# Performance work log

Measured on AMD Instinct MI355X. Metric: run time of the kernel, lower is better.

The kernel has to match this reference:

```python
import jax, jax.numpy as jnp
import numpy as np

N_NODES = 100000
E2 = 1600000
E3 = 1600000
ES = 100000
HID = 64


def _mlp_3x3(x_in, W1, b1, W2, b2):
    # x_in: [E, d_in] -> mobility [E, 3, 3]
    h = jax.nn.relu(x_in @ W1 + b1)
    out = h @ W2 + b2  # [E, 9]
    return out.reshape(-1, 3, 3)


def setup_inputs() -> dict:
    key = jax.random.key(0)
    ks = jax.random.split(key, 20)
    inp = {}
    inp["x"] = jax.random.normal(ks[0], (N_NODES, 3), dtype=jnp.float32)
    inp["edge_2body"] = jax.random.randint(ks[1], (2, E2), 0, N_NODES)
    inp["edge_3body"] = jax.random.randint(ks[2], (3, E3), 0, N_NODES)
    inp["edge_2bodySelf"] = jax.random.randint(ks[3], (2, ES), 0, N_NODES)
    inp["edge_1body"] = jax.random.randint(ks[4], (2, ES), 0, N_NODES)
    inp["edge_attr_2body"] = jax.random.normal(ks[5], (E2, 3), dtype=jnp.float32)
    inp["edge_attr_3body"] = jax.random.normal(ks[6], (E3, 3), dtype=jnp.float32)
    inp["edge_attr_2bodySelf"] = jax.random.normal(ks[7], (ES, 3), dtype=jnp.float32)
    inp["edge_attr_1body"] = jax.random.normal(ks[8], (ES, 3), dtype=jnp.float32)
    s = 0.1
    # nn_2body: 3 -> HID -> 9
    inp["W1_2b"] = jax.random.normal(ks[9], (3, HID), dtype=jnp.float32) * s
    inp["b1_2b"] = jnp.zeros((HID,), jnp.float32)
    inp["W2_2b"] = jax.random.normal(ks[10], (HID, 9), dtype=jnp.float32) * s
    inp["b2_2b"] = jnp.zeros((9,), jnp.float32)
    # nn_3body: 6 -> HID -> 9
    inp["W1_3b"] = jax.random.normal(ks[11], (6, HID), dtype=jnp.float32) * s
    inp["b1_3b"] = jnp.zeros((HID,), jnp.float32)
    inp["W2_3b"] = jax.random.normal(ks[12], (HID, 9), dtype=jnp.float32) * s
    inp["b2_3b"] = jnp.zeros((9,), jnp.float32)
    # nn_self: 3 -> HID -> 9
    inp["W1_s"] = jax.random.normal(ks[13], (3, HID), dtype=jnp.float32) * s
    inp["b1_s"] = jnp.zeros((HID,), jnp.float32)
    inp["W2_s"] = jax.random.normal(ks[14], (HID, 9), dtype=jnp.float32) * s
    inp["b2_s"] = jnp.zeros((9,), jnp.float32)
    return inp


def reference(x, edge_2body, edge_3body, edge_2bodySelf, edge_1body,
              edge_attr_2body, edge_attr_3body, edge_attr_2bodySelf, edge_attr_1body,
              W1_2b, b1_2b, W2_2b, b2_2b,
              W1_3b, b1_3b, W2_3b, b2_3b,
              W1_s, b1_s, W2_s, b2_s):
    n = x.shape[0]
    # ---- 2-body: gather -> MLP -> per-edge 3x3 matvec -> scatter-add ----
    d2 = x[edge_2body[0]] - x[edge_2body[1]]  # xj - xi, [E2,3]
    mob2 = _mlp_3x3(d2, W1_2b, b1_2b, W2_2b, b2_2b)
    y2 = jnp.einsum('eij,ej->ei', mob2, edge_attr_2body)
    v2 = jax.ops.segment_sum(y2, edge_2body[1], num_segments=n)
    # ---- 3-body ----
    xj = x[edge_3body[0]]
    xk = x[edge_3body[1]]
    xi = x[edge_3body[2]]
    d3 = jnp.concatenate((xk - xj, xi - xk), axis=1)  # [E3,6]
    mob3 = _mlp_3x3(d3, W1_3b, b1_3b, W2_3b, b2_3b)
    y3 = jnp.einsum('eij,ej->ei', mob3, edge_attr_3body)
    v3 = jax.ops.segment_sum(y3, edge_3body[2], num_segments=n)
    # ---- 2-body self ----
    ds = x[edge_2bodySelf[0]] - x[edge_2bodySelf[1]]
    mobs = _mlp_3x3(ds, W1_s, b1_s, W2_s, b2_s)
    ys = jnp.einsum('eij,ej->ei', mobs, edge_attr_2bodySelf)
    vs = jax.ops.segment_sum(ys, edge_2bodySelf[1], num_segments=n)
    # edge_1body / edge_attr_1body unused in original forward
    return v2 + v3 + vs
```

## Files before the change

kernel.cpp:

```cpp
#include <hip/hip_runtime.h>


constexpr int HIDDEN = 64;
constexpr int NB_MAX = 256;
constexpr int NPB_SHIFT = 9;
constexpr int NPB = 1 << NPB_SHIFT;
constexpr int TILE_F = NPB * 3;
constexpr int NET_SLOT = 1040;
constexpr int BLK = 256;
constexpr int KPT = 4;

typedef _Float16 h2_t __attribute__((ext_vector_type(2)));

__device__ __forceinline__ unsigned packh2(float a, float b) {
    auto h = __builtin_amdgcn_cvt_pkrtz(a, b);
    return __builtin_bit_cast(unsigned, h);
}
__device__ __forceinline__ float fdot2u(unsigned a, unsigned b, float c) {
    h2_t ha = __builtin_bit_cast(h2_t, a);
    h2_t hb = __builtin_bit_cast(h2_t, b);
#if __has_builtin(__builtin_amdgcn_fdot2)
    return __builtin_amdgcn_fdot2(ha, hb, c, false);
#else
    return fmaf((float)ha.x, (float)hb.x, fmaf((float)ha.y, (float)hb.y, c));
#endif
}


__global__ __launch_bounds__(256) void setup_kernel(
    const float* __restrict__ x, int n_nodes, float4* __restrict__ x4,
    int* __restrict__ gcount,
    const float* __restrict__ W1_2b, const float* __restrict__ b1_2b,
    const float* __restrict__ W2_2b, const float* __restrict__ b2_2b,
    const float* __restrict__ W1_s,  const float* __restrict__ b1_s,
    const float* __restrict__ W2_s,  const float* __restrict__ b2_s,
    const float* __restrict__ W1_3b, const float* __restrict__ b1_3b,
    const float* __restrict__ W2_3b, const float* __restrict__ b2_3b,
    unsigned* __restrict__ nets)
{
    const int blk = blockIdx.x;
    const int tid = threadIdx.x;
    if (blk < 3) {
        const float *W1, *b1, *W2, *b2; int din;
        if (blk == 0) { W1 = W1_2b; b1 = b1_2b; W2 = W2_2b; b2 = b2_2b; din = 3; }
        else if (blk == 1) { W1 = W1_s; b1 = b1_s; W2 = W2_s; b2 = b2_s; din = 3; }
        else { W1 = W1_3b; b1 = b1_3b; W2 = W2_3b; b2 = b2_3b; din = 6; }
        unsigned* slot = nets + blk * NET_SLOT;
        float* slotf = (float*)slot;
        if (tid < 32) {
            const int h2 = tid, hA = 2 * h2, hB = 2 * h2 + 1;
            if (din == 3) {
                unsigned* row = slot + h2 * 16;
                float* rowf = (float*)row;
                row[0] = packh2(W1[0 * HIDDEN + hA], W1[1 * HIDDEN + hA]);
                row[1] = packh2(W1[0 * HIDDEN + hB], W1[1 * HIDDEN + hB]);
                rowf[2] = b1[hA]; rowf[3] = b1[hB];
                rowf[4] = W1[2 * HIDDEN + hA]; rowf[5] = W1[2 * HIDDEN + hB];
                #pragma unroll
                for (int i = 0; i < 9; ++i)
                    row[6 + i] = packh2(W2[hA * 9 + i], W2[hB * 9 + i]);
                row[15] = 0;
            } else {
                unsigned* row = slot + h2 * 32;
                float* rowf = (float*)row;
                #pragma unroll
                for (int r = 0; r < 3; ++r) {
                    row[r]     = packh2(W1[(2 * r) * HIDDEN + hA], W1[(2 * r + 1) * HIDDEN + hA]);
                    row[3 + r] = packh2(W1[(2 * r) * HIDDEN + hB], W1[(2 * r + 1) * HIDDEN + hB]);
                }
                rowf[6] = b1[hA]; rowf[7] = b1[hB];
                #pragma unroll
                for (int i = 0; i < 9; ++i)
                    row[8 + i] = packh2(W2[hA * 9 + i], W2[hB * 9 + i]);
                #pragma unroll
                for (int i = 17; i < 20; ++i) row[i] = 0;
            }
        }
        if (tid >= 32 && tid < 41) slotf[1024 + (tid - 32)] = b2[tid - 32];
        if (blk == 0) gcount[tid] = 0;
    } else {
        int i = (blk - 3) * 256 + tid;
        if (i < n_nodes)
            x4[i] = make_float4(x[3 * i], x[3 * i + 1], x[3 * i + 2], 0.0f);
    }
}

__global__ __launch_bounds__(256) void p1_edge_kernel(
    const float4* __restrict__ x4,
    const int* __restrict__ e0, long long E0, const float* __restrict__ at0,
    const int* __restrict__ e1, long long E1, const float* __restrict__ at1,
    const int* __restrict__ e2, long long E2, const float* __restrict__ at2,
    int g0, int g1,
    const unsigned* __restrict__ nets,
    float4* __restrict__ records, int* __restrict__ gcount, int cap)
{
    static_assert(NB_MAX == BLK, "one reserve bin per thread");
    __shared__ __align__(16) unsigned s_net[1033];
    __shared__ int s_rank[NB_MAX];
    __shared__ int s_base[NB_MAX];

    const int gA = g0 + g1;
    const int gB = (int)gridDim.x - gA;
    const int mn = (gA < gB) ? gA : gB;
    int aidx = -1, b6 = -1;
    {
        const int idx = blockIdx.x;
        if (idx < 2 * mn) { if (idx & 1) b6 = idx >> 1; else aidx = idx >> 1; }
        else {
            const int r = idx - 2 * mn;
            if (gA > gB) aidx = mn + r; else b6 = mn + r;
        }
    }

    const int* edges; long long E; const float* attr;
    int bidx, nblk, din3;
    const unsigned* wp;
    if (aidx >= 0) {
        if (aidx < g0) { edges = e0; E = E0; attr = at0; bidx = aidx;      nblk = g0; din3 = 1; wp = nets; }
        else           { edges = e1; E = E1; attr = at1; bidx = aidx - g0; nblk = g1; din3 = 1; wp = nets + NET_SLOT; }
    } else             { edges = e2; E = E2; attr = at2; bidx = b6;        nblk = gB; din3 = 0; wp = nets + 2 * NET_SLOT; }

    const int tid = threadIdx.x;
    long long span = (E + nblk - 1) / nblk;
    span = (span + 1023) & ~1023LL;
    const long long lo = (long long)bidx * span;
    const long long hi = (lo + span < E) ? (lo + span) : E;
    if (lo >= E) return;

    const bool e_aligned = ((E & 3) == 0);

    s_rank[tid] = 0;
    const int nstage = din3 ? 512 : 1024;
    for (int i = tid; i < nstage; i += BLK) s_net[i] = wp[i];
    if (tid < 9) s_net[1024 + tid] = wp[1024 + tid];
    __syncthreads();

    const unsigned* w = s_net;
    const float* wf = (const float*)s_net;
    float b2r[9];
    #pragma unroll
    for (int i = 0; i < 9; ++i) b2r[i] = wf[1024 + i];

    const long long be = lo + (long long)tid * KPT;

    unsigned dp[KPT][3];
    float    d2s[KPT];
    float    a[KPT][3];
    int      dst[KPT];
    bool     valid[KPT];
    int      i0[KPT], i1[KPT], i2[KPT];

    const bool lane_live = (be < hi);
    const bool full = lane_live && e_aligned && (be + KPT <= hi);
    if (full) {
        int4 r0 = *(const int4*)(edges + be);
        int4 r1 = *(const int4*)(edges + E + be);
        i0[0] = r0.x; i0[1] = r0.y; i0[2] = r0.z; i0[3] = r0.w;
        i1[0] = r1.x; i1[1] = r1.y; i1[2] = r1.z; i1[3] = r1.w;
        if (!din3) {
            int4 r2 = *(const int4*)(edges + 2 * E + be);
            i2[0] = r2.x; i2[1] = r2.y; i2[2] = r2.z; i2[3] = r2.w;
        }
        float4 a0 = *(const float4*)(attr + 3 * be);
        float4 a1 = *(const float4*)(attr + 3 * be + 4);
        float4 a2 = *(const float4*)(attr + 3 * be + 8);
        a[0][0] = a0.x; a[0][1] = a0.y; a[0][2] = a0.z;
        a[1][0] = a0.w; a[1][1] = a1.x; a[1][2] = a1.y;
        a[2][0] = a1.z; a[2][1] = a1.w; a[2][2] = a2.x;
        a[3][0] = a2.y; a[3][1] = a2.z; a[3][2] = a2.w;
        #pragma unroll
        for (int u = 0; u < KPT; ++u) valid[u] = true;
    } else {
        #pragma unroll
        for (int u = 0; u < KPT; ++u) {
            long long e = be + u;
            valid[u] = lane_live && (e < hi);
            long long ee = valid[u] ? e : lo;
            i0[u] = edges[ee];
            i1[u] = edges[E + ee];
            if (!din3) i2[u] = edges[2 * E + ee];
            #pragma unroll
            for (int c = 0; c < 3; ++c) a[u][c] = attr[3 * ee + c];
        }
    }

    #pragma unroll
    for (int u = 0; u < KPT; ++u) {
        if (din3) {
            dst[u] = i1[u];
            float4 xs = x4[i0[u]];
            float4 xt = x4[i1[u]];
            dp[u][0] = packh2(xs.x - xt.x, xs.y - xt.y);
            d2s[u]   = xs.z - xt.z;
            dp[u][1] = 0; dp[u][2] = 0;
        } else {
            dst[u] = i2[u];
            float4 xj = x4[i0[u]];
            float4 xk = x4[i1[u]];
            float4 xi = x4[i2[u]];
            dp[u][0] = packh2(xk.x - xj.x, xk.y - xj.y);
            dp[u][1] = packh2(xk.z - xj.z, xi.x - xk.x);
            dp[u][2] = packh2(xi.y - xk.y, xi.z - xk.z);
            d2s[u] = 0.f;
        }
    }

    float acc[KPT][9];
    #pragma unroll
    for (int u = 0; u < KPT; ++u)
        #pragma unroll
        for (int i = 0; i < 9; ++i) acc[u][i] = b2r[i];

    if (din3) {
        #pragma unroll 2
        for (int hh2 = 0; hh2 < HIDDEN / 2; ++hh2) {
            const uint4* rq = (const uint4*)(w + (hh2 << 4));
            const uint4 q0 = rq[0], q1 = rq[1], q2 = rq[2], q3 = rq[3];
            const unsigned wA = q0.x;
            const unsigned wB = q0.y;
            const float bbA = __uint_as_float(q0.z);
            const float bbB = __uint_as_float(q0.w);
            const float wcA = __uint_as_float(q1.x);
            const float wcB = __uint_as_float(q1.y);
            const unsigned w2p[9] = {q1.z, q1.w, q2.x, q2.y, q2.z,
                                     q2.w, q3.x, q3.y, q3.z};
            #pragma unroll
            for (int u = 0; u < KPT; ++u) {
                float preA = fmaf(d2s[u], wcA, fdot2u(dp[u][0], wA, bbA));
                float preB = fmaf(d2s[u], wcB, fdot2u(dp[u][0], wB, bbB));
                unsigned h2 = packh2(fmaxf(preA, 0.f), fmaxf(preB, 0.f));
                #pragma unroll
                for (int i = 0; i < 9; ++i)
                    acc[u][i] = fdot2u(h2, w2p[i], acc[u][i]);
            }
        }
    } else {
        #pragma unroll 2
        for (int hh2 = 0; hh2 < HIDDEN / 2; ++hh2) {
            const uint4* rq = (const uint4*)(w + (hh2 << 5));
            const uint4 q0 = rq[0], q1 = rq[1], q2 = rq[2], q3 = rq[3];
            const unsigned q4x = w[(hh2 << 5) + 16];
            const unsigned wA0 = q0.x, wA1 = q0.y, wA2 = q0.z;
            const unsigned wB0 = q0.w, wB1 = q1.x, wB2 = q1.y;
            const float bbA = __uint_as_float(q1.z);
            const float bbB = __uint_as_float(q1.w);
            const unsigned w2p[9] = {q2.x, q2.y, q2.z, q2.w, q3.x,
                                     q3.y, q3.z, q3.w, q4x};
            #pragma unroll
            for (int u = 0; u < KPT; ++u) {
                float preA = fdot2u(dp[u][2], wA2,
                             fdot2u(dp[u][1], wA1,
                             fdot2u(dp[u][0], wA0, bbA)));
                float preB = fdot2u(dp[u][2], wB2,
                             fdot2u(dp[u][1], wB1,
                             fdot2u(dp[u][0], wB0, bbB)));
                unsigned h2 = packh2(fmaxf(preA, 0.f), fmaxf(preB, 0.f));
                #pragma unroll
                for (int i = 0; i < 9; ++i)
                    acc[u][i] = fdot2u(h2, w2p[i], acc[u][i]);
            }
        }
    }

    int rk[KPT]; int bb[KPT];
    #pragma unroll
    for (int u = 0; u < KPT; ++u) {
        if (valid[u]) {
            bb[u] = dst[u] >> NPB_SHIFT;
            rk[u] = atomicAdd(&s_rank[bb[u]], 1);
        }
    }
    __syncthreads();

    {
        int c = s_rank[tid];
        s_base[tid] = (c > 0) ? atomicAdd(&gcount[tid], c) : 0;
    }
    __syncthreads();

    #pragma unroll
    for (int u = 0; u < KPT; ++u) {
        if (!valid[u]) continue;
        float y0 = fmaf(acc[u][0], a[u][0], fmaf(acc[u][1], a[u][1], acc[u][2] * a[u][2]));
        float y1 = fmaf(acc[u][3], a[u][0], fmaf(acc[u][4], a[u][1], acc[u][5] * a[u][2]));
        float y2 = fmaf(acc[u][6], a[u][0], fmaf(acc[u][7], a[u][1], acc[u][8] * a[u][2]));
        int slot = s_base[bb[u]] + rk[u];
        if (slot < cap)
            records[(size_t)bb[u] * cap + slot] =
                make_float4(y0, y1, y2, __int_as_float(dst[u]));
    }
}

__global__ __launch_bounds__(1024) void p2_bucket(
    const float4* __restrict__ records, const int* __restrict__ gcount,
    int cap, int n_nodes, float* __restrict__ out)
{
    __shared__ float s_acc[TILE_F];
    const int b = blockIdx.x;
    const int tid = threadIdx.x;

    for (int i = tid; i < TILE_F; i += 1024) s_acc[i] = 0.0f;
    __syncthreads();

    int cnt = gcount[b];
    if (cnt > cap) cnt = cap;
    const float4* rb = records + (size_t)b * cap;
    for (int i = tid; i < cnt; i += 1024) {
        float4 r = rb[i];
        int loc = __float_as_int(r.w) - (b << NPB_SHIFT);
        atomicAdd(&s_acc[loc * 3 + 0], r.x);
        atomicAdd(&s_acc[loc * 3 + 1], r.y);
        atomicAdd(&s_acc[loc * 3 + 2], r.z);
    }
    __syncthreads();

    const int start = (b << NPB_SHIFT) * 3;
    const int end = min(n_nodes * 3, ((b + 1) << NPB_SHIFT) * 3);
    for (int i = start + tid; i < end; i += 1024)
        out[i] = s_acc[i - start];
}

template <int DIN, int KPTF>
__global__ __launch_bounds__(256) void edge_mlp_atomic(
    const float* __restrict__ x,
    const int* __restrict__ edges, long long E,
    const float* __restrict__ attr,
    const float* __restrict__ W1, const float* __restrict__ b1,
    const float* __restrict__ W2, const float* __restrict__ b2,
    float* __restrict__ out)
{
    const int tid = threadIdx.x;
    const long long base = (long long)blockIdx.x * (blockDim.x * KPTF) + tid;
    float d[KPTF][DIN]; float a[KPTF][3]; int dst[KPTF]; bool valid[KPTF];
    #pragma unroll
    for (int u = 0; u < KPTF; ++u) {
        long long e = base + (long long)u * blockDim.x;
        valid[u] = (e < E);
        long long ee = valid[u] ? e : 0;
        if constexpr (DIN == 3) {
            int s = edges[ee]; int t = edges[E + ee]; dst[u] = t;
            #pragma unroll
            for (int c = 0; c < 3; ++c)
                d[u][c] = x[3 * (long long)s + c] - x[3 * (long long)t + c];
        } else {
            int j = edges[ee]; int k = edges[E + ee]; int i = edges[2 * E + ee];
            dst[u] = i;
            #pragma unroll
            for (int c = 0; c < 3; ++c) {
                float xj = x[3 * (long long)j + c];
                float xk = x[3 * (long long)k + c];
                float xi = x[3 * (long long)i + c];
                d[u][c] = xk - xj; d[u][3 + c] = xi - xk;
            }
        }
        #pragma unroll
        for (int c = 0; c < 3; ++c) a[u][c] = attr[3 * ee + c];
    }
    float acc[KPTF][9];
    #pragma unroll
    for (int u = 0; u < KPTF; ++u)
        #pragma unroll
        for (int i = 0; i < 9; ++i) acc[u][i] = b2[i];
    #pragma unroll 4
    for (int hh = 0; hh < HIDDEN; ++hh) {
        const float bb = b1[hh];
        float w1r[DIN];
        #pragma unroll
        for (int r = 0; r < DIN; ++r) w1r[r] = W1[r * HIDDEN + hh];
        float w2r[9];
        #pragma unroll
        for (int i = 0; i < 9; ++i) w2r[i] = W2[hh * 9 + i];
        #pragma unroll
        for (int u = 0; u < KPTF; ++u) {
            float pre = bb;
            #pragma unroll
            for (int r = 0; r < DIN; ++r) pre = fmaf(d[u][r], w1r[r], pre);
            const float h = fmaxf(pre, 0.0f);
            #pragma unroll
            for (int i = 0; i < 9; ++i) acc[u][i] = fmaf(h, w2r[i], acc[u][i]);
        }
    }
    #pragma unroll
    for (int u = 0; u < KPTF; ++u) {
        if (!valid[u]) continue;
        float* o = out + 3 * (long long)dst[u];
        #pragma unroll
        for (int i = 0; i < 3; ++i) {
            float y = fmaf(acc[u][3 * i + 0], a[u][0],
                      fmaf(acc[u][3 * i + 1], a[u][1],
                           acc[u][3 * i + 2] * a[u][2]));
            atomicAdd(&o[i], y);
        }
    }
}

extern "C" void kernel_launch(void* const* d_in, const int* in_sizes, int n_in,
                              void* d_out, int out_size, void* d_ws, size_t ws_size,
                              hipStream_t stream)
{
    const float* x  = (const float*)d_in[0];
    const int*   e2 = (const int*)d_in[1];
    const int*   e3 = (const int*)d_in[2];
    const int*   es = (const int*)d_in[3];
    const float* a2 = (const float*)d_in[5];
    const float* a3 = (const float*)d_in[6];
    const float* as = (const float*)d_in[7];
    const float* W1_2b = (const float*)d_in[9];
    const float* b1_2b = (const float*)d_in[10];
    const float* W2_2b = (const float*)d_in[11];
    const float* b2_2b = (const float*)d_in[12];
    const float* W1_3b = (const float*)d_in[13];
    const float* b1_3b = (const float*)d_in[14];
    const float* W2_3b = (const float*)d_in[15];
    const float* b2_3b = (const float*)d_in[16];
    const float* W1_s  = (const float*)d_in[17];
    const float* b1_s  = (const float*)d_in[18];
    const float* W2_s  = (const float*)d_in[19];
    const float* b2_s  = (const float*)d_in[20];

    const long long E2 = in_sizes[1] / 2;
    const long long E3 = in_sizes[2] / 3;
    const long long ES = in_sizes[3] / 2;
    const long long Etot = E2 + E3 + ES;
    const int n_nodes = out_size / 3;
    const int nbuckets = (n_nodes + NPB - 1) >> NPB_SHIFT;

    float* out = (float*)d_out;

    const size_t off_nets = 1024;
    const size_t off_x4 = (off_nets + 3 * NET_SLOT * 4 + 255) & ~(size_t)255;
    const size_t x4_bytes = (size_t)n_nodes * sizeof(float4);
    const size_t off_rec = (off_x4 + x4_bytes + 255) & ~(size_t)255;

    long long mean_per_bucket = (Etot + nbuckets - 1) / nbuckets;
    long long min_cap = mean_per_bucket + 1600;
    long long cap_avail =
        ((long long)ws_size - (long long)off_rec) / ((long long)nbuckets * 16);

    constexpr int SPAN = 1024;
    int g0 = (int)((E2 + SPAN - 1) / SPAN);
    int g1 = (int)((ES + SPAN - 1) / SPAN);
    int g2g = (int)((E3 + SPAN - 1) / SPAN);

    if (nbuckets <= NB_MAX && cap_avail >= min_cap) {
        long long capL = min_cap + 4096;
        if (capL > cap_avail) capL = cap_avail;
        int cap = (int)capL;
        int* gcount = (int*)d_ws;
        unsigned* nets = (unsigned*)((char*)d_ws + off_nets);
        float4* x4 = (float4*)((char*)d_ws + off_x4);
        float4* records = (float4*)((char*)d_ws + off_rec);

        int nb_pad = (n_nodes + 255) / 256;
        setup_kernel<<<3 + nb_pad, 256, 0, stream>>>(
            x, n_nodes, x4, gcount,
            W1_2b, b1_2b, W2_2b, b2_2b,
            W1_s,  b1_s,  W2_s,  b2_s,
            W1_3b, b1_3b, W2_3b, b2_3b,
            nets);

        p1_edge_kernel<<<g0 + g1 + g2g, 256, 0, stream>>>(
            x4,
            e2, E2, a2,
            es, ES, as,
            e3, E3, a3,
            g0, g1,
            nets, records, gcount, cap);

        p2_bucket<<<nbuckets, 1024, 0, stream>>>(records, gcount, cap, n_nodes, out);
    } else {
        hipMemsetAsync(out, 0, (size_t)out_size * sizeof(float), stream);
        constexpr int FB_BLK = 256, FB_KPT = 4;
        const long long per_blk = (long long)FB_BLK * FB_KPT;
        int a2g = (int)((E2 + per_blk - 1) / per_blk);
        int a3g = (int)((E3 + per_blk - 1) / per_blk);
        int asg = (int)((ES + per_blk - 1) / per_blk);
        if (a2g > 0)
            edge_mlp_atomic<3, FB_KPT><<<a2g, FB_BLK, 0, stream>>>(
                x, e2, E2, a2, W1_2b, b1_2b, W2_2b, b2_2b, out);
        if (a3g > 0)
            edge_mlp_atomic<6, FB_KPT><<<a3g, FB_BLK, 0, stream>>>(
                x, e3, E3, a3, W1_3b, b1_3b, W2_3b, b2_3b, out);
        if (asg > 0)
            edge_mlp_atomic<3, FB_KPT><<<asg, FB_BLK, 0, stream>>>(
                x, es, ES, as, W1_s, b1_s, W2_s, b2_s, out);
    }
}
```

Measured before the change: 285.4 us.

## Double edges per thread and privatize bucket accumulators per wavefront

Raises the number of edges each thread handles in the bucketing kernel from 4 to 8, widening the vector loads and halving the grid, so each shared-memory weight load is reused across more edges. The hidden-layer loops lose their unroll-by-2 pragma to limit register growth. The bucket reduce kernel now gives each of the 16 wavefronts its own shared accumulator copy to cut LDS atomic contention, then sums the 16 copies when writing out. Costs are higher register pressure and roughly 96KB of LDS per block, which limits occupancy.

```diff
diff --git a/kernel.cpp b/kernel.cpp
--- a/kernel.cpp
+++ b/kernel.cpp
@@ -8,7 +8,7 @@
 constexpr int TILE_F = NPB * 3;
 constexpr int NET_SLOT = 1040;
 constexpr int BLK = 256;
-constexpr int KPT = 4;
+constexpr int KPT = 8;
 
 typedef _Float16 h2_t __attribute__((ext_vector_type(2)));
 
@@ -121,8 +121,9 @@
     } else             { edges = e2; E = E2; attr = at2; bidx = b6;        nblk = gB; din3 = 0; wp = nets + 2 * NET_SLOT; }
 
     const int tid = threadIdx.x;
+    constexpr int SPAN = BLK * KPT;
     long long span = (E + nblk - 1) / nblk;
-    span = (span + 1023) & ~1023LL;
+    span = (span + (SPAN - 1)) & ~(long long)(SPAN - 1);
     const long long lo = (long long)bidx * span;
     const long long hi = (lo + span < E) ? (lo + span) : E;
     if (lo >= E) return;
@@ -153,21 +154,25 @@
     const bool lane_live = (be < hi);
     const bool full = lane_live && e_aligned && (be + KPT <= hi);
     if (full) {
-        int4 r0 = *(const int4*)(edges + be);
-        int4 r1 = *(const int4*)(edges + E + be);
-        i0[0] = r0.x; i0[1] = r0.y; i0[2] = r0.z; i0[3] = r0.w;
-        i1[0] = r1.x; i1[1] = r1.y; i1[2] = r1.z; i1[3] = r1.w;
-        if (!din3) {
-            int4 r2 = *(const int4*)(edges + 2 * E + be);
-            i2[0] = r2.x; i2[1] = r2.y; i2[2] = r2.z; i2[3] = r2.w;
-        }
-        float4 a0 = *(const float4*)(attr + 3 * be);
-        float4 a1 = *(const float4*)(attr + 3 * be + 4);
-        float4 a2 = *(const float4*)(attr + 3 * be + 8);
-        a[0][0] = a0.x; a[0][1] = a0.y; a[0][2] = a0.z;
-        a[1][0] = a0.w; a[1][1] = a1.x; a[1][2] = a1.y;
-        a[2][0] = a1.z; a[2][1] = a1.w; a[2][2] = a2.x;
-        a[3][0] = a2.y; a[3][1] = a2.z; a[3][2] = a2.w;
+        #pragma unroll
+        for (int h = 0; h < 2; ++h) {
+            int4 r0 = *(const int4*)(edges + be + 4 * h);
+            int4 r1 = *(const int4*)(edges + E + be + 4 * h);
+            i0[4*h+0] = r0.x; i0[4*h+1] = r0.y; i0[4*h+2] = r0.z; i0[4*h+3] = r0.w;
+            i1[4*h+0] = r1.x; i1[4*h+1] = r1.y; i1[4*h+2] = r1.z; i1[4*h+3] = r1.w;
+            if (!din3) {
+                int4 r2 = *(const int4*)(edges + 2 * E + be + 4 * h);
+                i2[4*h+0] = r2.x; i2[4*h+1] = r2.y; i2[4*h+2] = r2.z; i2[4*h+3] = r2.w;
+            }
+        }
+        #pragma unroll
+        for (int q = 0; q < 6; ++q) {
+            float4 av = *(const float4*)(attr + 3 * be + 4 * q);
+            a[(4*q+0)/3][(4*q+0)%3] = av.x;
+            a[(4*q+1)/3][(4*q+1)%3] = av.y;
+            a[(4*q+2)/3][(4*q+2)%3] = av.z;
+            a[(4*q+3)/3][(4*q+3)%3] = av.w;
+        }
         #pragma unroll
         for (int u = 0; u < KPT; ++u) valid[u] = true;
     } else {
@@ -212,7 +217,6 @@
         for (int i = 0; i < 9; ++i) acc[u][i] = b2r[i];
 
     if (din3) {
-        #pragma unroll 2
         for (int hh2 = 0; hh2 < HIDDEN / 2; ++hh2) {
             const uint4* rq = (const uint4*)(w + (hh2 << 4));
             const uint4 q0 = rq[0], q1 = rq[1], q2 = rq[2], q3 = rq[3];
@@ -235,7 +239,6 @@
             }
         }
     } else {
-        #pragma unroll 2
         for (int hh2 = 0; hh2 < HIDDEN / 2; ++hh2) {
             const uint4* rq = (const uint4*)(w + (hh2 << 5));
             const uint4 q0 = rq[0], q1 = rq[1], q2 = rq[2], q3 = rq[3];
@@ -291,33 +294,41 @@
     }
 }
 
-__global__ __launch_bounds__(1024) void p2_bucket(
+__global__ __launch_bounds__(1024, 1) void p2_bucket(
     const float4* __restrict__ records, const int* __restrict__ gcount,
     int cap, int n_nodes, float* __restrict__ out)
 {
-    __shared__ float s_acc[TILE_F];
+    __shared__ float s_acc[16][TILE_F];
     const int b = blockIdx.x;
     const int tid = threadIdx.x;
-
-    for (int i = tid; i < TILE_F; i += 1024) s_acc[i] = 0.0f;
+    const int wv = tid >> 6;
+
+    for (int i = tid; i < 16 * TILE_F; i += 1024)
+        ((float*)s_acc)[i] = 0.0f;
     __syncthreads();
 
     int cnt = gcount[b];
     if (cnt > cap) cnt = cap;
     const float4* rb = records + (size_t)b * cap;
+    float* my = s_acc[wv];
     for (int i = tid; i < cnt; i += 1024) {
         float4 r = rb[i];
         int loc = __float_as_int(r.w) - (b << NPB_SHIFT);
-        atomicAdd(&s_acc[loc * 3 + 0], r.x);
-        atomicAdd(&s_acc[loc * 3 + 1], r.y);
-        atomicAdd(&s_acc[loc * 3 + 2], r.z);
+        atomicAdd(&my[loc * 3 + 0], r.x);
+        atomicAdd(&my[loc * 3 + 1], r.y);
+        atomicAdd(&my[loc * 3 + 2], r.z);
     }
     __syncthreads();
 
     const int start = (b << NPB_SHIFT) * 3;
     const int end = min(n_nodes * 3, ((b + 1) << NPB_SHIFT) * 3);
-    for (int i = start + tid; i < end; i += 1024)
-        out[i] = s_acc[i - start];
+    for (int i = start + tid; i < end; i += 1024) {
+        const int off = i - start;
+        float s = 0.0f;
+        #pragma unroll
+        for (int wvi = 0; wvi < 16; ++wvi) s += s_acc[wvi][off];
+        out[i] = s;
+    }
 }
 
 template <int DIN, int KPTF>
@@ -437,7 +448,7 @@
     long long cap_avail =
         ((long long)ws_size - (long long)off_rec) / ((long long)nbuckets * 16);
 
-    constexpr int SPAN = 1024;
+    constexpr int SPAN = BLK * KPT;
     int g0 = (int)((E2 + SPAN - 1) / SPAN);
     int g1 = (int)((ES + SPAN - 1) / SPAN);
     int g2g = (int)((E3 + SPAN - 1) / SPAN);
```

Result: slower. 300.9 us (+5.4%).
